# Optimization experiments

Hardware: AMD Instinct MI355X
Metric: run time of the kernel (lower is better)

## Reference

```python
import jax, jax.numpy as jnp
import numpy as np


def setup_inputs() -> dict:
    key = jax.random.key(0)
    ks = jax.random.split(key, 8)
    B, S, V, E, H = 64, 128, 8000, 256, 512
    scale = 0.05
    return {
        "inputs": jax.random.randint(ks[0], (B, S), 0, V, dtype=jnp.int64),
        "embedding": jax.random.normal(ks[1], (V, E), dtype=jnp.float32) * scale,
        "W_ih": jax.random.normal(ks[2], (4 * H, E), dtype=jnp.float32) * scale,
        "W_hh": jax.random.normal(ks[3], (4 * H, H), dtype=jnp.float32) * scale,
        "b_ih": jax.random.normal(ks[4], (4 * H,), dtype=jnp.float32) * scale,
        "b_hh": jax.random.normal(ks[5], (4 * H,), dtype=jnp.float32) * scale,
        "W_cls": jax.random.normal(ks[6], (V, H), dtype=jnp.float32) * scale,
        "b_cls": jax.random.normal(ks[7], (V,), dtype=jnp.float32) * scale,
    }


def reference(inputs, embedding, W_ih, W_hh, b_ih, b_hh, W_cls, b_cls):
    B, S = inputs.shape
    H = W_hh.shape[1]
    x = embedding[inputs]  # (B, S, E)
    # batch the input-to-hidden GEMM across all timesteps
    x_gates = jnp.einsum('bse,ge->bsg', x, W_ih) + b_ih + b_hh  # (B, S, 4H)

    def step(carry, xg):
        h, c = carry
        gates = xg + h @ W_hh.T  # (B, 4H)
        i, f, g, o = jnp.split(gates, 4, axis=-1)  # PyTorch LSTMCell gate order
        i = jax.nn.sigmoid(i)
        f = jax.nn.sigmoid(f)
        g = jnp.tanh(g)
        o = jax.nn.sigmoid(o)
        c = f * c + i * g
        h = o * jnp.tanh(c)
        return (h, c), h

    h0 = jnp.zeros((B, H), dtype=x.dtype)
    c0 = jnp.zeros((B, H), dtype=x.dtype)
    _, hs = jax.lax.scan(step, (h0, c0), jnp.swapaxes(x_gates, 0, 1))  # hs: (S, B, H)
    hidden = jnp.swapaxes(hs, 0, 1)  # (B, S, H)
    logits = jnp.einsum('bsh,vh->bsv', hidden, W_cls) + b_cls  # (B, S, V)
    y = jnp.transpose(logits, (0, 2, 1))  # (B, V, S)
    return jax.nn.log_softmax(y, axis=1)
```

## Files before the change

kernel.cpp:

```cpp
#include <hip/hip_runtime.h>


using u16   = unsigned short;
using u32   = unsigned int;
using u16x4 = __attribute__((ext_vector_type(4))) u16;
using u16x8 = __attribute__((ext_vector_type(8))) u16;
using bf16x8 = __attribute__((ext_vector_type(8))) __bf16;
using f32x4 = __attribute__((ext_vector_type(4))) float;

#define NB   64
#define NS   128
#define NV   8000
#define NVP  8192
#define NE   256
#define NH   512
#define NG   2048
#define NBS  8192
#define OUT_BSTRIDE 1024000
#define XG_SSTRIDE  131072

__device__ inline u16 f2bf(float f) {
    unsigned x = __builtin_bit_cast(unsigned, f);
    unsigned r = (x + 0x7FFFu + ((x >> 16) & 1u)) >> 16;
    return (u16)r;
}
__device__ inline float bf2f(u16 x) {
    u32 u = ((u32)x) << 16;
    return __builtin_bit_cast(float, u);
}

__device__ inline bf16x8 ld_frag(const u16* p) {
    u16x8 v = *(const u16x8*)p;
    return __builtin_bit_cast(bf16x8, v);
}

__device__ inline u32 load_llc(const u32* p) {
    u32 v;
    asm volatile("global_load_dword %0, %1, off sc0 sc1\n\t"
                 "s_waitcnt vmcnt(0)"
                 : "=v"(v) : "v"(p) : "memory");
    return v;
}
__device__ inline f32x4 load_llc16(const void* p) {
    f32x4 v;
    asm volatile("global_load_dwordx4 %0, %1, off sc0 sc1\n\t"
                 "s_waitcnt vmcnt(0)"
                 : "=v"(v) : "v"(p) : "memory");
    return v;
}
__device__ inline void store_llc(u32* p, u32 v) {
    asm volatile("global_store_dword %0, %1, off sc0 sc1"
                 :: "v"(p), "v"(v) : "memory");
}
__device__ inline void prefetch16(f32x4& d, const float* p) {
    asm volatile("global_load_dwordx4 %0, %1, off"
                 : "=v"(d) : "v"(p) : "memory");
}

__device__ inline void gload_lds16(const u16* g, u16* l) {
    __builtin_amdgcn_global_load_lds(
        (const __attribute__((address_space(1))) unsigned int*)(const void*)g,
        (__attribute__((address_space(3))) unsigned int*)(void*)l,
        16, 0, 0);
}

__device__ inline void quad_transpose(float v[4], int p) {
    float tb[4];
    #pragma unroll
    for (int q2 = 0; q2 < 4; ++q2) tb[q2] = __shfl_xor(v[q2 ^ 2], 2);
    #pragma unroll
    for (int q2 = 0; q2 < 4; ++q2) v[q2] = (((q2 ^ p) & 2) ? tb[q2] : v[q2]);
    #pragma unroll
    for (int q2 = 0; q2 < 4; ++q2) tb[q2] = __shfl_xor(v[q2 ^ 1], 1);
    #pragma unroll
    for (int q2 = 0; q2 < 4; ++q2) v[q2] = (((q2 ^ p) & 1) ? tb[q2] : v[q2]);
}

__device__ inline float lstm_cell(const float v[4], float& c) {
    float i_ = 1.f / (1.f + __expf(-v[0]));
    float f_ = 1.f / (1.f + __expf(-v[1]));
    float e2 = __expf(2.f * v[2]);
    float g_ = 1.f - 2.f / (e2 + 1.f);
    float o_ = 1.f / (1.f + __expf(-v[3]));
    c = f_ * c + i_ * g_;
    float e2c = __expf(2.f * c);
    return o_ * (1.f - 2.f / (e2c + 1.f));
}

__global__ void cvt_bf16(const float* __restrict__ s, u16* __restrict__ d, int n8) {
    const float4* s4 = (const float4*)s;
    for (int i = blockIdx.x * blockDim.x + threadIdx.x; i < n8;
         i += gridDim.x * blockDim.x) {
        float4 a = s4[2 * i], b = s4[2 * i + 1];
        u16x8 o;
        o[0] = f2bf(a.x); o[1] = f2bf(a.y); o[2] = f2bf(a.z); o[3] = f2bf(a.w);
        o[4] = f2bf(b.x); o[5] = f2bf(b.y); o[6] = f2bf(b.z); o[7] = f2bf(b.w);
        ((u16x8*)d)[i] = o;
    }
}

__global__ __launch_bounds__(256) void k1_xgates(
    const u16* __restrict__ Wih, const u16* __restrict__ emb,
    const int* __restrict__ toks,
    const float* __restrict__ bih, const float* __restrict__ bhh,
    float* __restrict__ xg)
{
    __shared__ u16x8 Al8[512];
    __shared__ u16x8 Bl8[512];
    u16* Al = (u16*)Al8;
    u16* Bl = (u16*)Bl8;

    const int t = threadIdx.x;
    const int lane = t & 63, w = t >> 6;
    const int wm = w >> 1, wn = w & 1;
    const int gtile = blockIdx.y * 128, mtile = blockIdx.x * 128;

    const int r0 = t >> 2, r1 = r0 + 64, q = t & 3;
    const int m0 = mtile + r0, m1 = mtile + r1;
    const int tok0 = toks[(m0 & 63) * NS + (m0 >> 6)];
    const int tok1 = toks[(m1 & 63) * NS + (m1 >> 6)];

    f32x4 acc[4][4];
    for (int i = 0; i < 4; ++i)
        for (int j = 0; j < 4; ++j) acc[i][j] = {0.f, 0.f, 0.f, 0.f};

    const int kc8 = (lane >> 4) * 8;
    for (int kk = 0; kk < 8; ++kk) {
        const int k0 = kk * 32;
        *(u16x8*)&Al[t * 8]         = *(const u16x8*)&Wih[(gtile + r0) * NE + k0 + q * 8];
        *(u16x8*)&Al[(t + 256) * 8] = *(const u16x8*)&Wih[(gtile + r1) * NE + k0 + q * 8];
        *(u16x8*)&Bl[t * 8]         = *(const u16x8*)&emb[tok0 * NE + k0 + q * 8];
        *(u16x8*)&Bl[(t + 256) * 8] = *(const u16x8*)&emb[tok1 * NE + k0 + q * 8];
        __syncthreads();
        bf16x8 af[4], bf[4];
        #pragma unroll
        for (int i = 0; i < 4; ++i) {
            af[i] = ld_frag(&Al[(wm * 64 + i * 16 + (lane & 15)) * 32 + kc8]);
            bf[i] = ld_frag(&Bl[(wn * 64 + i * 16 + (lane & 15)) * 32 + kc8]);
        }
        #pragma unroll
        for (int fi = 0; fi < 4; ++fi)
            #pragma unroll
            for (int fj = 0; fj < 4; ++fj)
                acc[fi][fj] = __builtin_amdgcn_mfma_f32_16x16x32_bf16(
                    af[fi], bf[fj], acc[fi][fj], 0, 0, 0);
        __syncthreads();
    }

    #pragma unroll
    for (int fi = 0; fi < 4; ++fi) {
        const int g0 = gtile + wm * 64 + fi * 16 + ((lane >> 4) << 2);
        const float4 v1 = *(const float4*)&bih[g0];
        const float4 v2 = *(const float4*)&bhh[g0];
        float badd[4] = {v1.x + v2.x, v1.y + v2.y, v1.z + v2.z, v1.w + v2.w};
        #pragma unroll
        for (int fj = 0; fj < 4; ++fj) {
            const int m = mtile + wn * 64 + fj * 16 + (lane & 15);
            const int b = m & 63, s = m >> 6;
            float* dst = &xg[s * XG_SSTRIDE + b];
            #pragma unroll
            for (int r = 0; r < 4; ++r)
                dst[(g0 + r) * 64] = acc[fi][fj][r] + badd[r];
        }
    }
}

#define LSTM_NBLK 64

__global__ __launch_bounds__(512, 2) void k2_lstm(
    const u16* __restrict__ Whh,
    const float* __restrict__ xg,
    u16* __restrict__ hbuf,
    u16* __restrict__ hidden,
    u32* __restrict__ flags)
{
    __shared__ __align__(16) u16 hl[16 * 528];

    const int t = threadIdx.x, lane = t & 63, w = t >> 6;
    const int bg = blockIdx.x >> 3, ug = blockIdx.x & 7;
    const int j = lane & 15;
    const int kc8 = (lane >> 4) * 8;

    const int ubase = ug * 64 + w * 8;
    const int grow0 = (j & 3) * 512 + ubase + (j >> 2);
    const int grow1 = grow0 + 4;

    bf16x8 bw0[16], bw1[16];
    #pragma unroll
    for (int kk = 0; kk < 16; ++kk) {
        bw0[kk] = ld_frag(&Whh[grow0 * NH + kk * 32 + kc8]);
        bw1[kk] = ld_frag(&Whh[grow1 * NH + kk * 32 + kc8]);
    }
    #pragma unroll
    for (int kk = 0; kk < 16; ++kk) {
        f32x4 w0 = __builtin_bit_cast(f32x4, bw0[kk]);
        f32x4 w1 = __builtin_bit_cast(f32x4, bw1[kk]);
        asm volatile("" : "+v"(w0), "+v"(w1));
        bw0[kk] = __builtin_bit_cast(bf16x8, w0);
        bw1[kk] = __builtin_bit_cast(bf16x8, w1);
    }

    {
        u16x8 z = {0, 0, 0, 0, 0, 0, 0, 0};
        *(u16x8*)&hl[(8 + (t >> 6)) * 528 + (t & 63) * 8] = z;
    }

    const int srow = t >> 6, scol = (t & 63) * 8;
    const int soff = (bg * 8 + srow) * NH + scol;
    u16* hl_w = &hl[srow * 528 + scol];

    const int p = lane & 3;
    const int q = (lane >> 2) & 3;
    const int batg = bg * 8 + (lane >> 4) * 4 + p;
    const int un0 = ubase + q;
    const bool act = lane < 32;
    const bool sl = act && ((lane & 4) == 0);

    const int xoff0 = grow0 * 64 + bg * 8 + (lane >> 4) * 4;
    const int xoff1 = grow1 * 64 + bg * 8 + (lane >> 4) * 4;

    f32x4 xv0 = {0, 0, 0, 0}, xv1 = {0, 0, 0, 0};
    f32x4 xn0 = {0, 0, 0, 0}, xn1 = {0, 0, 0, 0};
    if (act) {
        xv0 = *(const f32x4*)&xg[xoff0];
        xv1 = *(const f32x4*)&xg[xoff1];
    }
    float cA = 0.f, cB = 0.f;

    for (int step = 0; step < NS; ++step) {
        if (act && step + 1 < NS) {
            const float* xb = &xg[(step + 1) * XG_SSTRIDE];
            prefetch16(xn0, &xb[xoff0]);
            prefetch16(xn1, &xb[xoff1]);
        }
        if (step > 0 && lane < 8) {
            const u32* fp = &flags[(bg * 8 + lane) * 32];
            while ((int)load_llc(fp) < step) __builtin_amdgcn_s_sleep(1);
        }
        {
            f32x4 hv = load_llc16(&hbuf[(step & 1) * (NB * NH) + soff]);
            *(f32x4*)hl_w = hv;
        }
        __syncthreads();

        f32x4 a00 = {0, 0, 0, 0}, a01 = {0, 0, 0, 0};
        f32x4 a10 = {0, 0, 0, 0}, a11 = {0, 0, 0, 0};
        #pragma unroll
        for (int kk = 0; kk < 16; ++kk) {
            bf16x8 av = *(const bf16x8*)&hl[j * 528 + kk * 32 + kc8];
            if (kk & 1) {
                a01 = __builtin_amdgcn_mfma_f32_16x16x32_bf16(av, bw0[kk], a01, 0, 0, 0);
                a11 = __builtin_amdgcn_mfma_f32_16x16x32_bf16(av, bw1[kk], a11, 0, 0, 0);
            } else {
                a00 = __builtin_amdgcn_mfma_f32_16x16x32_bf16(av, bw0[kk], a00, 0, 0, 0);
                a10 = __builtin_amdgcn_mfma_f32_16x16x32_bf16(av, bw1[kk], a10, 0, 0, 0);
            }
        }

        float v0[4], v1[4];
        #pragma unroll
        for (int r = 0; r < 4; ++r) {
            v0[r] = a00[r] + a01[r] + xv0[r];
            v1[r] = a10[r] + a11[r] + xv1[r];
        }
        quad_transpose(v0, p);
        quad_transpose(v1, p);

        float h0 = lstm_cell(v0, cA);
        float h1 = lstm_cell(v1, cB);
        u32 hb0 = f2bf(h0), hb1 = f2bf(h1);
        u32 o0 = (u32)__shfl_xor((int)hb0, 4);
        u32 o1 = (u32)__shfl_xor((int)hb1, 4);
        u32 pr0 = hb0 | (o0 << 16);
        u32 pr1 = hb1 | (o1 << 16);

        if (sl) {
            u16* hn = hbuf + ((step & 1) ^ 1) * (NB * NH);
            store_llc((u32*)&hn[batg * NH + un0], pr0);
            store_llc((u32*)&hn[batg * NH + un0 + 4], pr1);
        }
        xv0 = xn0; xv1 = xn1;
        __syncthreads();

        if (step + 1 < NS && t == 0)
            store_llc(&flags[blockIdx.x * 32], (u32)(step + 1));

        if (sl) {
            *(u32*)&hidden[(batg * NS + step) * NH + un0] = pr0;
            *(u32*)&hidden[(batg * NS + step) * NH + un0 + 4] = pr1;
        }
    }
}

template <bool PACK16>
__global__ __launch_bounds__(256) void k3_cls(
    const u16* __restrict__ Wc, const u16* __restrict__ hid,
    const float* __restrict__ bcls,
    float* __restrict__ outf, u16* __restrict__ outb,
    float* __restrict__ lse)
{
    __shared__ __align__(16) u16 Al[128 * 32];
    __shared__ __align__(16) u16 Bl[128 * 32];
    __shared__ float red[2][128];

    const int t = threadIdx.x;
    const int lane = t & 63, w = t >> 6;
    const int wm = w >> 1, wn = w & 1;
    const int vtile = blockIdx.y * 128, mtile = blockIdx.x * 128;

    const int srow = w * 16 + (lane >> 2);
    const int scol = (lane & 3) * 8;
    const u16* gA = &Wc[(vtile + srow) * NH + scol];
    const u16* gB = &hid[(mtile + srow) * NH + scol];
    u16* lA0 = &Al[(w * 16) * 32];
    u16* lA1 = &Al[(w * 16 + 64) * 32];
    u16* lB0 = &Bl[(w * 16) * 32];
    u16* lB1 = &Bl[(w * 16 + 64) * 32];

    f32x4 acc[4][4];
    for (int i = 0; i < 4; ++i)
        for (int j2 = 0; j2 < 4; ++j2) acc[i][j2] = {0.f, 0.f, 0.f, 0.f};

    const int kc8 = (lane >> 4) * 8;
    for (int kk = 0; kk < 16; ++kk) {
        const int k0 = kk * 32;
        gload_lds16(gA + k0,           lA0);
        gload_lds16(gA + 64 * NH + k0, lA1);
        gload_lds16(gB + k0,           lB0);
        gload_lds16(gB + 64 * NH + k0, lB1);
        __syncthreads();
        bf16x8 mf[4], vf[4];
        #pragma unroll
        for (int i = 0; i < 4; ++i) {
            mf[i] = ld_frag(&Bl[(wm * 64 + i * 16 + (lane & 15)) * 32 + kc8]);
            vf[i] = ld_frag(&Al[(wn * 64 + i * 16 + (lane & 15)) * 32 + kc8]);
        }
        #pragma unroll
        for (int fi = 0; fi < 4; ++fi)
            #pragma unroll
            for (int fj = 0; fj < 4; ++fj)
                acc[fi][fj] = __builtin_amdgcn_mfma_f32_16x16x32_bf16(
                    mf[fi], vf[fj], acc[fi][fj], 0, 0, 0);
        __syncthreads();
    }

    float lsum[4][4];
    #pragma unroll
    for (int fi = 0; fi < 4; ++fi)
        #pragma unroll
        for (int r = 0; r < 4; ++r) lsum[fi][r] = 0.f;

    #pragma unroll
    for (int fj = 0; fj < 4; ++fj) {
        const int v = vtile + wn * 64 + fj * 16 + (lane & 15);
        const bool vok = (v < NV);
        const float bc = vok ? bcls[v] : 0.f;
        #pragma unroll
        for (int fi = 0; fi < 4; ++fi) {
            const int m = mtile + wm * 64 + fi * 16 + ((lane >> 4) << 2);
            const int b = m >> 7, s = m & 127;
            float lg[4];
            #pragma unroll
            for (int r = 0; r < 4; ++r) {
                lg[r] = acc[fi][fj][r] + bc;
                if (vok) lsum[fi][r] += __expf(lg[r]);
            }
            if (vok) {
                if (PACK16) {
                    u16x4 o = {f2bf(lg[0]), f2bf(lg[1]), f2bf(lg[2]), f2bf(lg[3])};
                    *(u16x4*)&outb[b * OUT_BSTRIDE + v * NS + s] = o;
                } else {
                    float4 o = {lg[0], lg[1], lg[2], lg[3]};
                    *(float4*)&outf[b * OUT_BSTRIDE + v * NS + s] = o;
                }
            }
        }
    }

    #pragma unroll
    for (int fi = 0; fi < 4; ++fi)
        #pragma unroll
        for (int r = 0; r < 4; ++r) {
            float sv = lsum[fi][r];
            sv += __shfl_xor(sv, 1);
            sv += __shfl_xor(sv, 2);
            sv += __shfl_xor(sv, 4);
            sv += __shfl_xor(sv, 8);
            lsum[fi][r] = sv;
        }
    if ((lane & 15) == 0) {
        #pragma unroll
        for (int fi = 0; fi < 4; ++fi)
            #pragma unroll
            for (int r = 0; r < 4; ++r)
                red[wn][wm * 64 + fi * 16 + ((lane >> 4) << 2) + r] = lsum[fi][r];
    }
    __syncthreads();
    if (t < 128) {
        const int m = mtile + t;
        atomicAdd(&lse[m], red[0][t] + red[1][t]);
    }
}

__global__ void k4_log(const float* __restrict__ lse, float* __restrict__ ll) {
    int i = blockIdx.x * 256 + threadIdx.x;
    if (i < NBS) ll[i] = logf(lse[i]);
}

__global__ void k5_norm(float* __restrict__ out, const float* __restrict__ ll) {
    const int total4 = NB * NV * NS / 4;
    float4* o4 = (float4*)out;
    for (int i = blockIdx.x * blockDim.x + threadIdx.x; i < total4;
         i += gridDim.x * blockDim.x) {
        const int i4 = i * 4;
        const int b = i4 / OUT_BSTRIDE;
        const int s = i4 & 127;
        float4 v = o4[i];
        const float4 l = *(const float4*)&ll[b * NS + s];
        v.x -= l.x; v.y -= l.y; v.z -= l.z; v.w -= l.w;
        o4[i] = v;
    }
}

__global__ void k5_bf16(float* __restrict__ out, const u16* __restrict__ lgb,
                        const float* __restrict__ ll) {
    const int total4 = NB * NV * NS / 4;
    float4* o4 = (float4*)out;
    const u16x4* l4 = (const u16x4*)lgb;
    for (int i = blockIdx.x * blockDim.x + threadIdx.x; i < total4;
         i += gridDim.x * blockDim.x) {
        const int i4 = i * 4;
        const int b = i4 / OUT_BSTRIDE;
        const int s = i4 & 127;
        u16x4 g = l4[i];
        const float4 l = *(const float4*)&ll[b * NS + s];
        float4 v;
        v.x = bf2f(g[0]) - l.x;
        v.y = bf2f(g[1]) - l.y;
        v.z = bf2f(g[2]) - l.z;
        v.w = bf2f(g[3]) - l.w;
        o4[i] = v;
    }
}

extern "C" void kernel_launch(void* const* d_in, const int* in_sizes, int n_in,
                              void* d_out, int out_size, void* d_ws, size_t ws_size,
                              hipStream_t stream) {
    const int*   toks   = (const int*)d_in[0];
    const float* emb_f  = (const float*)d_in[1];
    const float* Wih_f  = (const float*)d_in[2];
    const float* Whh_f  = (const float*)d_in[3];
    const float* bih    = (const float*)d_in[4];
    const float* bhh    = (const float*)d_in[5];
    const float* Wcls_f = (const float*)d_in[6];
    const float* bcls   = (const float*)d_in[7];
    float* out = (float*)d_out;
    char*  ws  = (char*)d_ws;

    u32*   flags  = (u32*)(ws + 0);
    float* lse    = (float*)(ws + 8192);
    float* loglse = (float*)(ws + 40960);
    u16*   hbuf   = (u16*)(ws + 73728);
    u16*   embb   = (u16*)(ws + 204800);
    u16*   wihb   = (u16*)(ws + 4300800);
    u16*   whhb   = (u16*)(ws + 5349376);
    u16*   wclsb  = (u16*)(ws + 7446528);
    u16*   hidden = (u16*)(ws + 15835136);
    u16*   lgb    = (u16*)(ws + 24223744);
    const bool bigws = ws_size >= (size_t)24223744 + (size_t)NB * NV * NS * 2;

    float* xg = out;

    hipMemsetAsync(ws, 0, 204800, stream);
    hipMemsetAsync((char*)wclsb + NV * NH * 2, 0, (NVP - NV) * NH * 2, stream);

    cvt_bf16<<<1024, 256, 0, stream>>>(emb_f,  embb,  NV * NE / 8);
    cvt_bf16<<<256,  256, 0, stream>>>(Wih_f,  wihb,  NG * NE / 8);
    cvt_bf16<<<512,  256, 0, stream>>>(Whh_f,  whhb,  NG * NH / 8);
    cvt_bf16<<<1024, 256, 0, stream>>>(Wcls_f, wclsb, NV * NH / 8);

    k1_xgates<<<dim3(64, 16), 256, 0, stream>>>(wihb, embb, toks, bih, bhh, xg);
    k2_lstm<<<LSTM_NBLK, 512, 0, stream>>>(whhb, xg, hbuf, hidden, flags);
    if (bigws) {
        k3_cls<true><<<dim3(64, 64), 256, 0, stream>>>(wclsb, hidden, bcls,
                                                       out, lgb, lse);
        k4_log<<<32, 256, 0, stream>>>(lse, loglse);
        k5_bf16<<<2048, 256, 0, stream>>>(out, lgb, loglse);
    } else {
        k3_cls<false><<<dim3(64, 64), 256, 0, stream>>>(wclsb, hidden, bcls,
                                                        out, lgb, lse);
        k4_log<<<32, 256, 0, stream>>>(lse, loglse);
        k5_norm<<<2048, 256, 0, stream>>>(out, loglse);
    }
}
```

Before: 607.1 us.

## Stage LSTM hidden state in LDS for vectorized stores; merge conversion kernels

The four fp32-to-bf16 weight conversion launches are merged into a single kernel, removing three launches. In the recurrent LSTM kernel, each wave writes its h values into a small LDS buffer. One wave then publishes them to the global exchange buffer with 16-byte LLC-coherent stores, waits for them to complete, and only then sets the step flag. A second wave writes the hidden output with 16-byte stores. This replaces many scattered 4-byte stores issued by every wave and places the flag after confirmed visibility, which should tighten the per-step cross-block handoff.

```diff
diff --git a/kernel.cpp b/kernel.cpp
--- a/kernel.cpp
+++ b/kernel.cpp
@@ -52,6 +52,10 @@
     asm volatile("global_store_dword %0, %1, off sc0 sc1"
                  :: "v"(p), "v"(v) : "memory");
 }
+__device__ inline void store_llc16(void* p, u16x8 v) {
+    asm volatile("global_store_dwordx4 %0, %1, off sc0 sc1"
+                 :: "v"(p), "v"(__builtin_bit_cast(f32x4, v)) : "memory");
+}
 __device__ inline void prefetch16(f32x4& d, const float* p) {
     asm volatile("global_load_dwordx4 %0, %1, off"
                  : "=v"(d) : "v"(p) : "memory");
@@ -87,15 +91,25 @@
     return o_ * (1.f - 2.f / (e2c + 1.f));
 }
 
-__global__ void cvt_bf16(const float* __restrict__ s, u16* __restrict__ d, int n8) {
-    const float4* s4 = (const float4*)s;
-    for (int i = blockIdx.x * blockDim.x + threadIdx.x; i < n8;
+__global__ void cvt_all(const float* __restrict__ e,  const float* __restrict__ wi,
+                        const float* __restrict__ wh, const float* __restrict__ wc,
+                        u16* __restrict__ de,  u16* __restrict__ dwi,
+                        u16* __restrict__ dwh, u16* __restrict__ dwc) {
+    const int N0 = NV * NE / 8, N1 = NG * NE / 8, N2 = NG * NH / 8, N3 = NV * NH / 8;
+    const int total = N0 + N1 + N2 + N3;
+    for (int i = blockIdx.x * blockDim.x + threadIdx.x; i < total;
          i += gridDim.x * blockDim.x) {
-        float4 a = s4[2 * i], b = s4[2 * i + 1];
+        const float* s; u16* d; int j;
+        if (i < N0)                { s = e;  d = de;  j = i; }
+        else if (i < N0 + N1)      { s = wi; d = dwi; j = i - N0; }
+        else if (i < N0 + N1 + N2) { s = wh; d = dwh; j = i - N0 - N1; }
+        else                       { s = wc; d = dwc; j = i - N0 - N1 - N2; }
+        const float4* s4 = (const float4*)s;
+        float4 a = s4[2 * j], b = s4[2 * j + 1];
         u16x8 o;
         o[0] = f2bf(a.x); o[1] = f2bf(a.y); o[2] = f2bf(a.z); o[3] = f2bf(a.w);
         o[4] = f2bf(b.x); o[5] = f2bf(b.y); o[6] = f2bf(b.z); o[7] = f2bf(b.w);
-        ((u16x8*)d)[i] = o;
+        ((u16x8*)d)[j] = o;
     }
 }
 
@@ -175,6 +189,7 @@
     u32* __restrict__ flags)
 {
     __shared__ __align__(16) u16 hl[16 * 528];
+    __shared__ __align__(16) u16 hex[8 * 64];
 
     const int t = threadIdx.x, lane = t & 63, w = t >> 6;
     const int bg = blockIdx.x >> 3, ug = blockIdx.x & 7;
@@ -211,8 +226,7 @@
 
     const int p = lane & 3;
     const int q = (lane >> 2) & 3;
-    const int batg = bg * 8 + (lane >> 4) * 4 + p;
-    const int un0 = ubase + q;
+    const int bl = (lane >> 4) * 4 + p;
     const bool act = lane < 32;
     const bool sl = act && ((lane & 4) == 0);
 
@@ -271,23 +285,29 @@
         u32 hb0 = f2bf(h0), hb1 = f2bf(h1);
         u32 o0 = (u32)__shfl_xor((int)hb0, 4);
         u32 o1 = (u32)__shfl_xor((int)hb1, 4);
-        u32 pr0 = hb0 | (o0 << 16);
-        u32 pr1 = hb1 | (o1 << 16);
 
         if (sl) {
-            u16* hn = hbuf + ((step & 1) ^ 1) * (NB * NH);
-            store_llc((u32*)&hn[batg * NH + un0], pr0);
-            store_llc((u32*)&hn[batg * NH + un0 + 4], pr1);
+            u32* hx = (u32*)hex;
+            hx[bl * 32 + (w * 8 + q) / 2]       = hb0 | (o0 << 16);
+            hx[bl * 32 + (w * 8 + q + 4) / 2]   = hb1 | (o1 << 16);
         }
         xv0 = xn0; xv1 = xn1;
         __syncthreads();
 
-        if (step + 1 < NS && t == 0)
-            store_llc(&flags[blockIdx.x * 32], (u32)(step + 1));
-
-        if (sl) {
-            *(u32*)&hidden[(batg * NS + step) * NH + un0] = pr0;
-            *(u32*)&hidden[(batg * NS + step) * NH + un0 + 4] = pr1;
+        if (w == 0) {
+            if (step + 1 < NS) {
+                u16x8 hv = *(const u16x8*)&hex[lane * 8];
+                store_llc16(&hbuf[((step + 1) & 1) * (NB * NH)
+                                  + (bg * 8 + (lane >> 3)) * NH
+                                  + ug * 64 + (lane & 7) * 8], hv);
+                asm volatile("s_waitcnt vmcnt(0)" ::: "memory");
+                if (lane == 0)
+                    store_llc(&flags[blockIdx.x * 32], (u32)(step + 1));
+            }
+        } else if (w == 1) {
+            u16x8 hv = *(const u16x8*)&hex[lane * 8];
+            *(u16x8*)&hidden[((bg * 8 + (lane >> 3)) * NS + step) * NH
+                             + ug * 64 + (lane & 7) * 8] = hv;
         }
     }
 }
@@ -474,10 +494,8 @@
     hipMemsetAsync(ws, 0, 204800, stream);
     hipMemsetAsync((char*)wclsb + NV * NH * 2, 0, (NVP - NV) * NH * 2, stream);
 
-    cvt_bf16<<<1024, 256, 0, stream>>>(emb_f,  embb,  NV * NE / 8);
-    cvt_bf16<<<256,  256, 0, stream>>>(Wih_f,  wihb,  NG * NE / 8);
-    cvt_bf16<<<512,  256, 0, stream>>>(Whh_f,  whhb,  NG * NH / 8);
-    cvt_bf16<<<1024, 256, 0, stream>>>(Wcls_f, wclsb, NV * NH / 8);
+    cvt_all<<<2048, 256, 0, stream>>>(emb_f, Wih_f, Whh_f, Wcls_f,
+                                      embb, wihb, whhb, wclsb);
 
     k1_xgates<<<dim3(64, 16), 256, 0, stream>>>(wihb, embb, toks, bih, bhh, xg);
     k2_lstm<<<LSTM_NBLK, 512, 0, stream>>>(whhb, xg, hbuf, hidden, flags);
```

Result: slower. 660.3 us (+8.8%).
